# Optimization experiments

Hardware: AMD Instinct MI355X
Metric: run time of the kernel (lower is better)

## Reference

```python
import jax, jax.numpy as jnp
import numpy as np

B, N, DIM = 4, 2048, 512
HEADS, DIM_HEAD = 8, 64
HIDDEN = HEADS * DIM_HEAD  # == DIM


def _rotary(t):
    # t: [b, h, n, d]; interleaved rotary (rotary-embedding-torch style), theta=10000
    n, d = t.shape[-2], t.shape[-1]
    inv_freq = 1.0 / (10000.0 ** (jnp.arange(0, d, 2, dtype=jnp.float32) / d))  # [d/2]
    freqs = jnp.arange(n, dtype=jnp.float32)[:, None] * inv_freq[None, :]        # [n, d/2]
    freqs = jnp.repeat(freqs, 2, axis=-1)                                        # [n, d]
    cos, sin = jnp.cos(freqs), jnp.sin(freqs)
    x1, x2 = t[..., ::2], t[..., 1::2]
    rot = jnp.stack((-x2, x1), axis=-1).reshape(t.shape)  # rotate_half, interleaved
    return t * cos + rot * sin


def setup_inputs() -> dict:
    key = jax.random.key(0)
    k1, k2, k3, k4 = jax.random.split(key, 4)
    x = jax.random.normal(k1, (B, N, DIM), dtype=jnp.float32)
    pos_bias = jax.random.normal(k2, (HEADS, N, N), dtype=jnp.float32)
    W_qkv = jax.random.normal(k3, (DIM, 3 * HIDDEN), dtype=jnp.float32) * (DIM ** -0.5)
    W_out = jax.random.normal(k4, (HIDDEN, DIM), dtype=jnp.float32) * (HIDDEN ** -0.5)
    return {"x": x, "pos_bias": pos_bias, "W_qkv": W_qkv, "W_out": W_out}


def reference(x, pos_bias, W_qkv, W_out):
    b, n, _ = x.shape
    qkv = x @ W_qkv                                   # [b, n, 3*h*d]
    q, k, v = jnp.split(qkv, 3, axis=-1)

    def to_heads(t):
        return t.reshape(b, n, HEADS, DIM_HEAD).transpose(0, 2, 1, 3)  # [b,h,n,d]

    q = to_heads(q) * (DIM_HEAD ** -0.5)
    k = to_heads(k)
    v = to_heads(v)
    q = _rotary(q)
    k = _rotary(k)
    sim = jnp.einsum('bhid,bhjd->bhij', q, k) + pos_bias[None]  # [b,h,n,n]
    attn = jax.nn.softmax(sim, axis=-1)                          # stable softmax (== amax-subtract + softmax)
    out = jnp.einsum('bhij,bhjd->bhid', attn, v)
    out = out.transpose(0, 2, 1, 3).reshape(b, n, HIDDEN)
    return out @ W_out
```

## Files before the change

kernel.cpp:

```cpp
#include <hip/hip_runtime.h>
#include <hip/hip_bf16.h>

#define DEV static __device__ __forceinline__

typedef __attribute__((ext_vector_type(8))) short s16x8;
typedef __attribute__((ext_vector_type(16))) float f32x16;

DEV float bf2f(short s) {
    unsigned u = ((unsigned)(unsigned short)s) << 16;
    union { unsigned u; float f; } c; c.u = u; return c.f;
}
DEV short f2bf(float f) {
    union { float f; unsigned u; } c; c.f = f;
    unsigned u = c.u;
    unsigned r = (u + 0x7FFFu + ((u >> 16) & 1u)) >> 16;
    return (short)r;
}

DEV f32x16 mfma(s16x8 a, s16x8 b, f32x16 c) {
    return __builtin_amdgcn_mfma_f32_32x32x16_bf16(a, b, c, 0, 0, 0);
}

typedef const __attribute__((address_space(1))) unsigned gu32;
typedef __attribute__((address_space(3))) unsigned lu32;
DEV void gll16(const float* g, float* l) {
    __builtin_amdgcn_global_load_lds((gu32*)g, (lu32*)l, 16, 0, 0);
}

__global__ void cvt_f32_bf16(const float* __restrict__ src,
                             short* __restrict__ dst, int n) {
    int i = (blockIdx.x * blockDim.x + threadIdx.x) * 4;
    if (i >= n) return;
    float4 v = *(const float4*)(src + i);
    short4 o;
    o.x = f2bf(v.x); o.y = f2bf(v.y); o.z = f2bf(v.z); o.w = f2bf(v.w);
    *(short4*)(dst + i) = o;
}

__global__ void rotab(float2* __restrict__ tab) {
    int idx = blockIdx.x * 256 + threadIdx.x;
    int n = idx >> 5, f = idx & 31;
    float inv = expf(-0.2878231366f * (float)f);
    float a = (float)n * inv;
    tab[idx] = make_float2(cosf(a), sinf(a));
}

__global__ void ktransf(const float* __restrict__ src, short* __restrict__ dst,
                        int R, int C) {
    __shared__ __align__(16) short t[32][33];
    int tx = threadIdx.x & 31, ty = threadIdx.x >> 5;
    int r0 = blockIdx.y * 32, c0 = blockIdx.x * 32;
    for (int i = 0; i < 32; i += 8)
        t[ty + i][tx] = f2bf(src[(size_t)(r0 + ty + i) * C + c0 + tx]);
    __syncthreads();
    for (int i = 0; i < 32; i += 8)
        dst[(size_t)(c0 + ty + i) * R + r0 + tx] = t[tx][ty + i];
}

__global__ __launch_bounds__(256) void gemm_qkv(
    const short* __restrict__ X, const short* __restrict__ WT,
    const float2* __restrict__ rtab,
    short* __restrict__ qws, short* __restrict__ kws, short* __restrict__ vt) {
    int wave = threadIdx.x >> 6, lane = threadIdx.x & 63;
    int l31 = lane & 31, lh = lane >> 5;
    int mw = blockIdx.x * 128 + (wave >> 1) * 64;
    int nw = blockIdx.y * 128 + (wave & 1) * 64;
    f32x16 acc[2][2] = {};
    const short* ap = X + (size_t)(mw + l31) * 512 + lh * 8;
    const short* bp = WT + (size_t)(nw + l31) * 512 + lh * 8;
#pragma unroll 4
    for (int k = 0; k < 512; k += 16) {
        s16x8 a0 = *(const s16x8*)(ap + k);
        s16x8 a1 = *(const s16x8*)(ap + 32 * 512 + k);
        s16x8 b0 = *(const s16x8*)(bp + k);
        s16x8 b1 = *(const s16x8*)(bp + 32 * 512 + k);
        acc[0][0] = mfma(a0, b0, acc[0][0]);
        acc[0][1] = mfma(a0, b1, acc[0][1]);
        acc[1][0] = mfma(a1, b0, acc[1][0]);
        acc[1][1] = mfma(a1, b1, acc[1][1]);
    }
#pragma unroll
    for (int ib = 0; ib < 2; ib++)
#pragma unroll
        for (int jb = 0; jb < 2; jb++) {
            int col = nw + jb * 32 + l31;
            int t = col >> 9;
            int cid = col & 511;
            int h = cid >> 6, d = cid & 63;
#pragma unroll
            for (int r = 0; r < 16; r++) {
                int row = (r & 3) + 8 * (r >> 2) + 4 * lh;
                int gm = mw + ib * 32 + row;
                int b = gm >> 11, n = gm & 2047;
                float v = acc[ib][jb][r];
                if (t == 0) v *= 0.125f;
                if (t < 2) {
                    float pv = __shfl_xor(v, 1);
                    float2 cs = rtab[n * 32 + (d >> 1)];
                    float o = (d & 1) ? (v * cs.x + pv * cs.y)
                                      : (v * cs.x - pv * cs.y);
                    short* dst = (t == 0) ? qws : kws;
                    dst[((size_t)(b * 8 + h) * 2048 + n) * 64 + d] = f2bf(o);
                } else {
                    vt[((size_t)(b * 8 + h) * 64 + d) * 2048 + n] = f2bf(v);
                }
            }
        }
}

__global__ __launch_bounds__(64) void attn(
    const short* __restrict__ qws, const short* __restrict__ kws,
    const short* __restrict__ vt, const float* __restrict__ bias,
    short* __restrict__ ows) {
    __shared__ __align__(16) short pls[32 * 64];
    __shared__ __align__(16) float blds[2][32][64];
    int lane = threadIdx.x;
    int l31 = lane & 31, lh = lane >> 5;
    int bid = blockIdx.x;
    int h = bid & 7;
    int b = (bid >> 3) & 3;
    int q0 = (bid >> 5) * 32;
    int bh = b * 8 + h;

    const short* qp = qws + ((size_t)bh * 2048 + q0 + l31) * 64 + lh * 8;
    s16x8 qf[4];
#pragma unroll
    for (int c = 0; c < 4; c++) qf[c] = *(const s16x8*)(qp + c * 16);

    f32x16 oa[2] = {};
    float lsum[16];
#pragma unroll
    for (int r = 0; r < 16; r++) lsum[r] = 0.f;
    short* pw = &pls[0];

    const float* bbase = bias + ((size_t)h * 2048 + q0) * 2048;
    int grow = lane >> 4;
    int gcol = (lane & 15) * 4;

#pragma unroll
    for (int j = 0; j < 8; j++)
        gll16(bbase + (size_t)(4 * j + grow) * 2048 + gcol, &blds[0][4 * j][0]);

    for (int kt = 0; kt < 32; kt++) {
        int kb = kt * 64;
        int p = kt & 1;
        const short* kp = kws + ((size_t)bh * 2048 + kb + l31) * 64 + lh * 8;
        s16x8 k0[4], k1[4];
#pragma unroll
        for (int c = 0; c < 4; c++) {
            k0[c] = *(const s16x8*)(kp + c * 16);
            k1[c] = *(const s16x8*)(kp + 32 * 64 + c * 16);
        }
        __builtin_amdgcn_sched_barrier(0);
        if (kt < 31) {
            const float* bnx = bbase + (size_t)(kt + 1) * 64;
#pragma unroll
            for (int j = 0; j < 8; j++)
                gll16(bnx + (size_t)(4 * j + grow) * 2048 + gcol,
                      &blds[p ^ 1][4 * j][0]);
        }
        f32x16 s0 = {}, s1 = {};
#pragma unroll
        for (int c = 0; c < 4; c++) {
            s0 = mfma(qf[c], k0[c], s0);
            s1 = mfma(qf[c], k1[c], s1);
        }
        asm volatile("s_waitcnt vmcnt(16)" ::: "memory");
        __builtin_amdgcn_sched_barrier(0);
#pragma unroll
        for (int r = 0; r < 16; r++) {
            int row = (r & 3) + 8 * (r >> 2) + 4 * lh;
            float e0 = __expf(s0[r] + blds[p][row][l31]);
            float e1 = __expf(s1[r] + blds[p][row][32 + l31]);
            lsum[r] += e0 + e1;
            int sw = (row & 7) << 3;
            pw[row * 64 + (l31 ^ sw)] = f2bf(e0);
            pw[row * 64 + ((32 + l31) ^ sw)] = f2bf(e1);
        }
        const short* vp = vt + ((size_t)bh * 64 + l31) * 2048 + kb + lh * 8;
#pragma unroll
        for (int c = 0; c < 4; c++) {
            s16x8 pf = *(const s16x8*)(
                pw + l31 * 64 + ((c * 16 + lh * 8) ^ ((l31 & 7) << 3)));
            s16x8 v0f = *(const s16x8*)(vp + c * 16);
            s16x8 v1f = *(const s16x8*)(vp + (size_t)32 * 2048 + c * 16);
            oa[0] = mfma(pf, v0f, oa[0]);
            oa[1] = mfma(pf, v1f, oa[1]);
        }
    }
#pragma unroll
    for (int r = 0; r < 16; r++) {
        float s = lsum[r];
#pragma unroll
        for (int off = 16; off >= 1; off >>= 1)
            s += __shfl_xor(s, off);
        float inv = 1.f / s;
        int row = (r & 3) + 8 * (r >> 2) + 4 * lh;
        size_t o0 = ((size_t)(b * 2048 + q0 + row) * 8 + h) * 64;
        ows[o0 + l31] = f2bf(oa[0][r] * inv);
        ows[o0 + 32 + l31] = f2bf(oa[1][r] * inv);
    }
}

__global__ __launch_bounds__(256) void gemm_out(
    const short* __restrict__ O, const short* __restrict__ WT,
    float* __restrict__ out) {
    int wave = threadIdx.x >> 6, lane = threadIdx.x & 63;
    int l31 = lane & 31, lh = lane >> 5;
    int m0 = blockIdx.x * 128 + (wave >> 1) * 64;
    int n0 = blockIdx.y * 128 + (wave & 1) * 64;
    f32x16 acc[2][2] = {};
    const short* ap = O + (size_t)(m0 + l31) * 512 + lh * 8;
    const short* bp = WT + (size_t)(n0 + l31) * 512 + lh * 8;
#pragma unroll 4
    for (int k = 0; k < 512; k += 16) {
        s16x8 a0 = *(const s16x8*)(ap + k);
        s16x8 a1 = *(const s16x8*)(ap + 32 * 512 + k);
        s16x8 b0 = *(const s16x8*)(bp + k);
        s16x8 b1 = *(const s16x8*)(bp + 32 * 512 + k);
        acc[0][0] = mfma(a0, b0, acc[0][0]);
        acc[0][1] = mfma(a0, b1, acc[0][1]);
        acc[1][0] = mfma(a1, b0, acc[1][0]);
        acc[1][1] = mfma(a1, b1, acc[1][1]);
    }
#pragma unroll
    for (int ib = 0; ib < 2; ib++)
#pragma unroll
        for (int jb = 0; jb < 2; jb++)
#pragma unroll
            for (int r = 0; r < 16; r++) {
                int row = (r & 3) + 8 * (r >> 2) + 4 * lh;
                out[(size_t)(m0 + ib * 32 + row) * 512 + n0 + jb * 32 + l31] =
                    acc[ib][jb][r];
            }
}

extern "C" void kernel_launch(void* const* d_in, const int* in_sizes, int n_in,
                              void* d_out, int out_size, void* d_ws,
                              size_t ws_size, hipStream_t stream) {
    const float* x    = (const float*)d_in[0];
    const float* bias = (const float*)d_in[1];
    const float* wqkv = (const float*)d_in[2];
    const float* wout = (const float*)d_in[3];
    float* out = (float*)d_out;

    char* ws = (char*)d_ws;
    short* xbf   = (short*)ws;
    short* wqkvT = xbf + 4194304;
    short* woutT = wqkvT + 786432;
    short* qws   = woutT + 262144;
    short* kws   = qws + 4194304;
    short* vt    = kws + 4194304;
    short* ows   = vt + 4194304;
    float2* rtab = (float2*)(ows + 4194304);

    cvt_f32_bf16<<<4096, 256, 0, stream>>>(x, xbf, 4194304);
    rotab<<<256, 256, 0, stream>>>(rtab);
    ktransf<<<dim3(1536 / 32, 512 / 32), 256, 0, stream>>>(wqkv, wqkvT, 512, 1536);
    ktransf<<<dim3(512 / 32, 512 / 32), 256, 0, stream>>>(wout, woutT, 512, 512);
    gemm_qkv<<<dim3(64, 12), 256, 0, stream>>>(xbf, wqkvT, rtab, qws, kws, vt);
    attn<<<2048, 64, 0, stream>>>(qws, kws, vt, bias, ows);
    gemm_out<<<dim3(64, 4), 256, 0, stream>>>(ows, woutT, out);
}
```

Baseline: 418.1 us.

## Compute transposed scores so softmax probabilities stay in registers, dropping LDS

Swaps the MFMA operand order so each lane holds scores for one query column, which lets the bias rows be read straight from global memory as float4 per lane instead of staged through LDS with global_load_lds double buffering. Probabilities are packed to bf16 with v_cvt_pk_bf16_f32 and rearranged into the PV A-operand layout with v_permlane32_swap, removing the LDS write/read round trip for P. Row sums become per-lane scalars that need only one cross-half shuffle, and the normalisation is broadcast with __shfl. The trade-off is more VGPR pressure and no explicit prefetch overlap for the bias loads.

```diff
diff --git a/kernel.cpp b/kernel.cpp
--- a/kernel.cpp
+++ b/kernel.cpp
@@ -5,6 +5,7 @@
 
 typedef __attribute__((ext_vector_type(8))) short s16x8;
 typedef __attribute__((ext_vector_type(16))) float f32x16;
+typedef __attribute__((ext_vector_type(4))) unsigned u32x4;
 
 DEV float bf2f(short s) {
     unsigned u = ((unsigned)(unsigned short)s) << 16;
@@ -21,10 +22,13 @@
     return __builtin_amdgcn_mfma_f32_32x32x16_bf16(a, b, c, 0, 0, 0);
 }
 
-typedef const __attribute__((address_space(1))) unsigned gu32;
-typedef __attribute__((address_space(3))) unsigned lu32;
-DEV void gll16(const float* g, float* l) {
-    __builtin_amdgcn_global_load_lds((gu32*)g, (lu32*)l, 16, 0, 0);
+DEV unsigned cvtpk(float lo, float hi) {
+    unsigned r;
+    asm("v_cvt_pk_bf16_f32 %0, %1, %2" : "=v"(r) : "v"(lo), "v"(hi));
+    return r;
+}
+DEV void pl32swap(unsigned& a, unsigned& b) {
+    asm volatile("v_permlane32_swap_b32 %0, %1" : "+v"(a), "+v"(b));
 }
 
 __global__ void cvt_f32_bf16(const float* __restrict__ src,
@@ -112,8 +116,6 @@
     const short* __restrict__ qws, const short* __restrict__ kws,
     const short* __restrict__ vt, const float* __restrict__ bias,
     short* __restrict__ ows) {
-    __shared__ __align__(16) short pls[32 * 64];
-    __shared__ __align__(16) float blds[2][32][64];
     int lane = threadIdx.x;
     int l31 = lane & 31, lh = lane >> 5;
     int bid = blockIdx.x;
@@ -128,77 +130,81 @@
     for (int c = 0; c < 4; c++) qf[c] = *(const s16x8*)(qp + c * 16);
 
     f32x16 oa[2] = {};
-    float lsum[16];
-#pragma unroll
-    for (int r = 0; r < 16; r++) lsum[r] = 0.f;
-    short* pw = &pls[0];
-
-    const float* bbase = bias + ((size_t)h * 2048 + q0) * 2048;
-    int grow = lane >> 4;
-    int gcol = (lane & 15) * 4;
-
-#pragma unroll
-    for (int j = 0; j < 8; j++)
-        gll16(bbase + (size_t)(4 * j + grow) * 2048 + gcol, &blds[0][4 * j][0]);
+    float ls0 = 0.f, ls1 = 0.f, ls2 = 0.f, ls3 = 0.f;
+
+    const float* browp = bias + ((size_t)h * 2048 + q0 + l31) * 2048;
+    const short* kbase = kws + ((size_t)bh * 2048 + l31) * 64 + lh * 8;
+    const short* vbase = vt + ((size_t)bh * 64 + l31) * 2048 + lh * 8;
 
     for (int kt = 0; kt < 32; kt++) {
         int kb = kt * 64;
-        int p = kt & 1;
-        const short* kp = kws + ((size_t)bh * 2048 + kb + l31) * 64 + lh * 8;
+        const short* kp = kbase + (size_t)kb * 64;
         s16x8 k0[4], k1[4];
 #pragma unroll
         for (int c = 0; c < 4; c++) {
             k0[c] = *(const s16x8*)(kp + c * 16);
             k1[c] = *(const s16x8*)(kp + 32 * 64 + c * 16);
         }
-        __builtin_amdgcn_sched_barrier(0);
-        if (kt < 31) {
-            const float* bnx = bbase + (size_t)(kt + 1) * 64;
-#pragma unroll
-            for (int j = 0; j < 8; j++)
-                gll16(bnx + (size_t)(4 * j + grow) * 2048 + gcol,
-                      &blds[p ^ 1][4 * j][0]);
+        float bae[16], bbe[16];
+#pragma unroll
+        for (int g = 0; g < 4; g++) {
+            float4 ta = *(const float4*)(browp + kb + 8 * g + 4 * lh);
+            float4 tb = *(const float4*)(browp + kb + 32 + 8 * g + 4 * lh);
+            bae[4 * g + 0] = ta.x; bae[4 * g + 1] = ta.y;
+            bae[4 * g + 2] = ta.z; bae[4 * g + 3] = ta.w;
+            bbe[4 * g + 0] = tb.x; bbe[4 * g + 1] = tb.y;
+            bbe[4 * g + 2] = tb.z; bbe[4 * g + 3] = tb.w;
         }
         f32x16 s0 = {}, s1 = {};
 #pragma unroll
         for (int c = 0; c < 4; c++) {
-            s0 = mfma(qf[c], k0[c], s0);
-            s1 = mfma(qf[c], k1[c], s1);
-        }
-        asm volatile("s_waitcnt vmcnt(16)" ::: "memory");
-        __builtin_amdgcn_sched_barrier(0);
+            s0 = mfma(k0[c], qf[c], s0);
+            s1 = mfma(k1[c], qf[c], s1);
+        }
+        const short* vp = vbase + kb;
+        s16x8 v0f[4], v1f[4];
+#pragma unroll
+        for (int c = 0; c < 4; c++) {
+            v0f[c] = *(const s16x8*)(vp + c * 16);
+            v1f[c] = *(const s16x8*)(vp + (size_t)32 * 2048 + c * 16);
+        }
+        float p0[16], p1[16];
 #pragma unroll
         for (int r = 0; r < 16; r++) {
-            int row = (r & 3) + 8 * (r >> 2) + 4 * lh;
-            float e0 = __expf(s0[r] + blds[p][row][l31]);
-            float e1 = __expf(s1[r] + blds[p][row][32 + l31]);
-            lsum[r] += e0 + e1;
-            int sw = (row & 7) << 3;
-            pw[row * 64 + (l31 ^ sw)] = f2bf(e0);
-            pw[row * 64 + ((32 + l31) ^ sw)] = f2bf(e1);
-        }
-        const short* vp = vt + ((size_t)bh * 64 + l31) * 2048 + kb + lh * 8;
-#pragma unroll
-        for (int c = 0; c < 4; c++) {
-            s16x8 pf = *(const s16x8*)(
-                pw + l31 * 64 + ((c * 16 + lh * 8) ^ ((l31 & 7) << 3)));
-            s16x8 v0f = *(const s16x8*)(vp + c * 16);
-            s16x8 v1f = *(const s16x8*)(vp + (size_t)32 * 2048 + c * 16);
-            oa[0] = mfma(pf, v0f, oa[0]);
-            oa[1] = mfma(pf, v1f, oa[1]);
-        }
-    }
+            float e0 = __expf(s0[r] + bae[r]);
+            float e1 = __expf(s1[r] + bbe[r]);
+            p0[r] = e0; p1[r] = e1;
+            if ((r & 3) == 0) ls0 += e0 + e1;
+            else if ((r & 3) == 1) ls1 += e0 + e1;
+            else if ((r & 3) == 2) ls2 += e0 + e1;
+            else ls3 += e0 + e1;
+        }
+#pragma unroll
+        for (int c = 0; c < 4; c++) {
+            const float* ps = (c < 2) ? p0 : p1;
+            int gb = (c & 1) * 2;
+            unsigned x0 = cvtpk(ps[4 * gb + 0], ps[4 * gb + 1]);
+            unsigned x1 = cvtpk(ps[4 * (gb + 1) + 0], ps[4 * (gb + 1) + 1]);
+            unsigned y0 = cvtpk(ps[4 * gb + 2], ps[4 * gb + 3]);
+            unsigned y1 = cvtpk(ps[4 * (gb + 1) + 2], ps[4 * (gb + 1) + 3]);
+            pl32swap(x0, x1);
+            pl32swap(y0, y1);
+            u32x4 uw = {x0, y0, x1, y1};
+            union { u32x4 u; s16x8 s; } pa; pa.u = uw;
+            oa[0] = mfma(pa.s, v0f[c], oa[0]);
+            oa[1] = mfma(pa.s, v1f[c], oa[1]);
+        }
+    }
+    float lsum = (ls0 + ls1) + (ls2 + ls3);
+    lsum += __shfl_xor(lsum, 32);
+    float inv = 1.f / lsum;
 #pragma unroll
     for (int r = 0; r < 16; r++) {
-        float s = lsum[r];
-#pragma unroll
-        for (int off = 16; off >= 1; off >>= 1)
-            s += __shfl_xor(s, off);
-        float inv = 1.f / s;
-        int row = (r & 3) + 8 * (r >> 2) + 4 * lh;
-        size_t o0 = ((size_t)(b * 2048 + q0 + row) * 8 + h) * 64;
-        ows[o0 + l31] = f2bf(oa[0][r] * inv);
-        ows[o0 + 32 + l31] = f2bf(oa[1][r] * inv);
+        int cr = (r & 3) + 8 * (r >> 2) + 4 * lh;
+        float invr = __shfl(inv, cr);
+        size_t o0 = ((size_t)(b * 2048 + q0 + cr) * 8 + h) * 64;
+        ows[o0 + l31] = f2bf(oa[0][r] * invr);
+        ows[o0 + 32 + l31] = f2bf(oa[1][r] * invr);
     }
 }
 
```

New measurement: 456.2 us. 1.09x slower.
